# Kernel tuning notes

Hardware: AMD Instinct MI355X
Metric: run time of the kernel (lower is better)

The kernel has to match this reference:

```python
import jax, jax.numpy as jnp
import numpy as np

IN_FEATS = 602
N_HIDDEN = 256
N_CLASSES = 41
N_SRC0 = 292864   # block-1 src nodes (2-hop neighborhood)
N_DST0 = 11264    # block-1 dst == block-0 src (1-hop neighborhood)
N_DST1 = 1024     # seeds
FAN0 = 25         # neighbors per dst in block applied by layer 0
FAN1 = 10         # neighbors per dst in block applied by layer 1


def setup_inputs() -> dict:
    key = jax.random.key(0)
    ks = jax.random.split(key, 9)
    x = jax.random.normal(ks[0], (N_SRC0, IN_FEATS), dtype=jnp.float32)
    src_idx0 = jax.random.randint(ks[1], (N_DST0 * FAN0,), 0, N_SRC0)
    src_idx1 = jax.random.randint(ks[2], (N_DST1 * FAN1,), 0, N_DST0)
    s0 = 1.0 / np.sqrt(IN_FEATS)
    s1 = 1.0 / np.sqrt(N_HIDDEN)
    W_self0 = jax.random.uniform(ks[3], (IN_FEATS, N_HIDDEN), jnp.float32, -s0, s0)
    W_neigh0 = jax.random.uniform(ks[4], (IN_FEATS, N_HIDDEN), jnp.float32, -s0, s0)
    b0 = jnp.zeros((N_HIDDEN,), jnp.float32)
    W_self1 = jax.random.uniform(ks[5], (N_HIDDEN, N_CLASSES), jnp.float32, -s1, s1)
    W_neigh1 = jax.random.uniform(ks[6], (N_HIDDEN, N_CLASSES), jnp.float32, -s1, s1)
    b1 = jnp.zeros((N_CLASSES,), jnp.float32)
    return {"x": x, "W_self0": W_self0, "W_neigh0": W_neigh0, "b0": b0,
            "W_self1": W_self1, "W_neigh1": W_neigh1, "b1": b1,
            "src_idx0": src_idx0, "src_idx1": src_idx1}


def _sage_layer(h_src, h_dst, src_idx, fanout, W_self, W_neigh, b):
    # mean aggregation over exactly `fanout` sampled neighbors per dst node
    n_dst = h_dst.shape[0]
    h_neigh = h_src[src_idx].reshape(n_dst, fanout, -1).mean(axis=1)
    return h_dst @ W_self + h_neigh @ W_neigh + b


def reference(x, W_self0, W_neigh0, b0, W_self1, W_neigh1, b1, src_idx0, src_idx1):
    # layer 0: [N_SRC0, in] -> [N_DST0, hidden], relu; dropout is identity (eval mode)
    h = jax.nn.relu(_sage_layer(x, x[:N_DST0], src_idx0, FAN0, W_self0, W_neigh0, b0))
    # layer 1: [N_DST0, hidden] -> [N_DST1, classes], no activation
    out = _sage_layer(h, h[:N_DST1], src_idx1, FAN1, W_self1, W_neigh1, b1)
    return out
```

## Files before the change

kernel.cpp:

```cpp
#include <hip/hip_runtime.h>
#include <hip/hip_bf16.h>

#define IN_FEATS 602
#define N_HIDDEN 256
#define N_CLASSES 41
#define N_SRC0 292864
#define N_DST0 11264
#define N_DST1 1024
#define FAN0 25
#define FAN1 10
#define KPAD 1216

typedef __attribute__((ext_vector_type(4))) float f32x4;
typedef __attribute__((ext_vector_type(8))) short bf16x8;

static __device__ __forceinline__ unsigned pack_bf16x2(float lo, float hi) {
    unsigned a = __float_as_uint(lo);
    unsigned b = __float_as_uint(hi);
    a = (a + 0x7fffu + ((a >> 16) & 1u)) >> 16;
    b = (b + 0x7fffu + ((b >> 16) & 1u)) >> 16;
    return (a & 0xffffu) | (b << 16);
}

__global__ __launch_bounds__(256) void agg0_kernel(
    const float* __restrict__ x,
    const int* __restrict__ idx,
    __hip_bfloat16* __restrict__ A)
{
    const int wave = threadIdx.x >> 6;
    const int lane = threadIdx.x & 63;
    const int d = blockIdx.x * 4 + wave;

    __shared__ int sidx[4][FAN0];
    if (lane < FAN0) sidx[wave][lane] = idx[d * FAN0 + lane];
    __syncthreads();

    unsigned* Arow = (unsigned*)(A + (size_t)d * KPAD);
    const float* xself = x + (size_t)d * IN_FEATS;

    if (lane < 6) Arow[602 + lane] = 0u;

    float accx[5], accy[5];
    #pragma unroll
    for (int c = 0; c < 5; ++c) { accx[c] = 0.f; accy[c] = 0.f; }

    #pragma unroll 5
    for (int n = 0; n < FAN0; ++n) {
        const float* xr = x + (size_t)sidx[wave][n] * IN_FEATS;
        #pragma unroll
        for (int c = 0; c < 5; ++c) {
            const int f = c * 128 + lane * 2;
            if (f < IN_FEATS) {
                const float2 v = *(const float2*)&xr[f];
                accx[c] += v.x; accy[c] += v.y;
            }
        }
    }

    #pragma unroll
    for (int c = 0; c < 5; ++c) {
        const int f = c * 128 + lane * 2;
        if (f < IN_FEATS) {
            const int f2 = f >> 1;
            const float2 sv = *(const float2*)&xself[f];
            Arow[f2] = pack_bf16x2(sv.x, sv.y);
            *(unsigned*)((char*)Arow + 1204 + f2 * 4) =
                pack_bf16x2(accx[c] * (1.0f / FAN0), accy[c] * (1.0f / FAN0));
        }
    }
}

__global__ __launch_bounds__(256) void wprep_kernel(
    const float* __restrict__ Ws,
    const float* __restrict__ Wn,
    __hip_bfloat16* __restrict__ Wt)
{
    __shared__ float tile[32][33];
    const int k0 = blockIdx.x * 32, n0 = blockIdx.y * 32;
    const int tx = threadIdx.x & 31, ty = threadIdx.x >> 5;

    #pragma unroll
    for (int i = 0; i < 4; ++i) {
        const int k = k0 + ty + i * 8;
        const int n = n0 + tx;
        float v = 0.f;
        if (k < IN_FEATS)            v = Ws[(size_t)k * N_HIDDEN + n];
        else if (k < 2 * IN_FEATS)   v = Wn[(size_t)(k - IN_FEATS) * N_HIDDEN + n];
        tile[ty + i * 8][tx] = v;
    }
    __syncthreads();
    #pragma unroll
    for (int i = 0; i < 4; ++i) {
        const int n = n0 + ty + i * 8;
        const int k = k0 + tx;
        Wt[(size_t)n * KPAD + k] = __float2bfloat16(tile[tx][ty + i * 8]);
    }
}

#define BKK 64
#define LDSW 72

__global__ __launch_bounds__(256) void gemm0_mfma(
    const __hip_bfloat16* __restrict__ A,
    const __hip_bfloat16* __restrict__ Wt,
    const float* __restrict__ bias,
    float* __restrict__ h)
{
    __shared__ __hip_bfloat16 As[64 * LDSW];
    __shared__ __hip_bfloat16 Bs[64 * LDSW];

    const int tid  = threadIdx.x;
    const int lane = tid & 63;
    const int wave = tid >> 6;
    const int wm = wave >> 1, wn = wave & 1;
    const int g = lane >> 4, r = lane & 15;
    const int m0 = blockIdx.y * 64, n0 = blockIdx.x * 64;

    const int srow = tid >> 2;
    const int sc   = (tid & 3) * 16;

    const size_t a_off = (size_t)(m0 + srow) * KPAD + sc;
    const size_t b_off = (size_t)(n0 + srow) * KPAD + sc;

    f32x4 acc[2][2] = {};

    for (int k0 = 0; k0 < KPAD; k0 += BKK) {
        *(float4*)&As[srow * LDSW + sc]     = *(const float4*)&A[a_off + k0];
        *(float4*)&As[srow * LDSW + sc + 8] = *(const float4*)&A[a_off + k0 + 8];
        *(float4*)&Bs[srow * LDSW + sc]     = *(const float4*)&Wt[b_off + k0];
        *(float4*)&Bs[srow * LDSW + sc + 8] = *(const float4*)&Wt[b_off + k0 + 8];
        __syncthreads();

        #pragma unroll
        for (int kh = 0; kh < 2; ++kh) {
            const bf16x8 af0 = *(const bf16x8*)&As[(wm * 32 +      r) * LDSW + kh * 32 + g * 8];
            const bf16x8 af1 = *(const bf16x8*)&As[(wm * 32 + 16 + r) * LDSW + kh * 32 + g * 8];
            const bf16x8 bf0 = *(const bf16x8*)&Bs[(wn * 32 +      r) * LDSW + kh * 32 + g * 8];
            const bf16x8 bf1 = *(const bf16x8*)&Bs[(wn * 32 + 16 + r) * LDSW + kh * 32 + g * 8];

            acc[0][0] = __builtin_amdgcn_mfma_f32_16x16x32_bf16(af0, bf0, acc[0][0], 0, 0, 0);
            acc[0][1] = __builtin_amdgcn_mfma_f32_16x16x32_bf16(af0, bf1, acc[0][1], 0, 0, 0);
            acc[1][0] = __builtin_amdgcn_mfma_f32_16x16x32_bf16(af1, bf0, acc[1][0], 0, 0, 0);
            acc[1][1] = __builtin_amdgcn_mfma_f32_16x16x32_bf16(af1, bf1, acc[1][1], 0, 0, 0);
        }
        __syncthreads();
    }

    #pragma unroll
    for (int mh = 0; mh < 2; ++mh)
        #pragma unroll
        for (int nh = 0; nh < 2; ++nh) {
            const int col = n0 + wn * 32 + nh * 16 + r;
            const float bv = bias[col];
            #pragma unroll
            for (int j = 0; j < 4; ++j) {
                const int row = m0 + wm * 32 + mh * 16 + g * 4 + j;
                const float v = acc[mh][nh][j] + bv;
                h[(size_t)row * N_HIDDEN + col] = fmaxf(v, 0.f);
            }
        }
}

__global__ __launch_bounds__(256) void tail_kernel(
    const float* __restrict__ h,
    const int* __restrict__ idx1,
    const float* __restrict__ Ws,
    const float* __restrict__ Wn,
    const float* __restrict__ b,
    float* __restrict__ out)
{
    const int w = threadIdx.x >> 6;
    const int lane = threadIdx.x & 63;
    const int d = blockIdx.x * 4 + w;

    __shared__ float hd[4][N_HIDDEN];
    __shared__ float hn[4][N_HIDDEN];
    __shared__ int sidx[4][FAN1];
    if (lane < FAN1) sidx[w][lane] = idx1[d * FAN1 + lane];
    __syncthreads();

    {
        const int k0 = lane * 4;
        const float4 self = *(const float4*)&h[(size_t)d * N_HIDDEN + k0];
        float ax = 0.f, ay = 0.f, az = 0.f, aw = 0.f;
        #pragma unroll
        for (int i = 0; i < FAN1; ++i) {
            const float4 v = *(const float4*)&h[(size_t)sidx[w][i] * N_HIDDEN + k0];
            ax += v.x; ay += v.y; az += v.z; aw += v.w;
        }
        *(float4*)&hd[w][k0] = self;
        hn[w][k0 + 0] = ax * (1.0f / FAN1);
        hn[w][k0 + 1] = ay * (1.0f / FAN1);
        hn[w][k0 + 2] = az * (1.0f / FAN1);
        hn[w][k0 + 3] = aw * (1.0f / FAN1);
    }
    __syncthreads();

    if (lane < N_CLASSES) {
        const int n = lane;
        float a0 = b[n], a1 = 0.f, a2 = 0.f, a3 = 0.f;
        #pragma unroll 4
        for (int k = 0; k < N_HIDDEN; k += 4) {
            a0 += hd[w][k + 0] * Ws[(k + 0) * N_CLASSES + n] + hn[w][k + 0] * Wn[(k + 0) * N_CLASSES + n];
            a1 += hd[w][k + 1] * Ws[(k + 1) * N_CLASSES + n] + hn[w][k + 1] * Wn[(k + 1) * N_CLASSES + n];
            a2 += hd[w][k + 2] * Ws[(k + 2) * N_CLASSES + n] + hn[w][k + 2] * Wn[(k + 2) * N_CLASSES + n];
            a3 += hd[w][k + 3] * Ws[(k + 3) * N_CLASSES + n] + hn[w][k + 3] * Wn[(k + 3) * N_CLASSES + n];
        }
        out[(size_t)d * N_CLASSES + n] = a0 + a1 + a2 + a3;
    }
}

extern "C" void kernel_launch(void* const* d_in, const int* in_sizes, int n_in,
                              void* d_out, int out_size, void* d_ws, size_t ws_size,
                              hipStream_t stream) {
    const float* x       = (const float*)d_in[0];
    const float* Wself0  = (const float*)d_in[1];
    const float* Wneigh0 = (const float*)d_in[2];
    const float* b0      = (const float*)d_in[3];
    const float* Wself1  = (const float*)d_in[4];
    const float* Wneigh1 = (const float*)d_in[5];
    const float* b1      = (const float*)d_in[6];
    const int*   idx0    = (const int*)d_in[7];
    const int*   idx1    = (const int*)d_in[8];
    float* out = (float*)d_out;

    __hip_bfloat16* Abf = (__hip_bfloat16*)d_ws;
    __hip_bfloat16* Wt  = Abf + (size_t)N_DST0 * KPAD;
    float*          h   = (float*)(Wt + (size_t)N_HIDDEN * KPAD);

    wprep_kernel<<<dim3(KPAD / 32, N_HIDDEN / 32), 256, 0, stream>>>(Wself0, Wneigh0, Wt);
    agg0_kernel<<<N_DST0 / 4, 256, 0, stream>>>(x, idx0, Abf);
    gemm0_mfma<<<dim3(N_HIDDEN / 64, N_DST0 / 64), 256, 0, stream>>>(Abf, Wt, b0, h);
    tail_kernel<<<N_DST1 / 4, 256, 0, stream>>>(h, idx1, Wself1, Wneigh1, b1, out);
}
```

Before: 232.2 us.

## Merge weight prep into aggregation launch and double-buffer GEMM LDS tiles

Folds the weight transpose/convert kernel into the aggregation kernel as extra blocks, saving one launch and letting both run concurrently. The GEMM switches to double-buffered LDS with register prefetch of the next K tile, which drops one barrier per iteration and overlaps global loads with MFMA work. It also remaps the 1D block index so consecutive blocks share A row tiles across the N columns, aiming for better L2 reuse. The cost is double the LDS footprint and more registers in the GEMM.

```diff
diff --git a/kernel.cpp b/kernel.cpp
--- a/kernel.cpp
+++ b/kernel.cpp
@@ -10,6 +10,8 @@
 #define FAN0 25
 #define FAN1 10
 #define KPAD 1216
+#define NAGG (N_DST0 / 4)
+#define NWP ((KPAD / 32) * (N_HIDDEN / 32))
 
 typedef __attribute__((ext_vector_type(4))) float f32x4;
 typedef __attribute__((ext_vector_type(8))) short bf16x8;
@@ -22,78 +24,81 @@
     return (a & 0xffffu) | (b << 16);
 }
 
-__global__ __launch_bounds__(256) void agg0_kernel(
+__global__ __launch_bounds__(256) void prep_kernel(
     const float* __restrict__ x,
     const int* __restrict__ idx,
-    __hip_bfloat16* __restrict__ A)
+    const float* __restrict__ Ws,
+    const float* __restrict__ Wn,
+    __hip_bfloat16* __restrict__ A,
+    __hip_bfloat16* __restrict__ Wt)
 {
-    const int wave = threadIdx.x >> 6;
-    const int lane = threadIdx.x & 63;
-    const int d = blockIdx.x * 4 + wave;
-
-    __shared__ int sidx[4][FAN0];
-    if (lane < FAN0) sidx[wave][lane] = idx[d * FAN0 + lane];
-    __syncthreads();
-
-    unsigned* Arow = (unsigned*)(A + (size_t)d * KPAD);
-    const float* xself = x + (size_t)d * IN_FEATS;
-
-    if (lane < 6) Arow[602 + lane] = 0u;
-
-    float accx[5], accy[5];
-    #pragma unroll
-    for (int c = 0; c < 5; ++c) { accx[c] = 0.f; accy[c] = 0.f; }
-
-    #pragma unroll 5
-    for (int n = 0; n < FAN0; ++n) {
-        const float* xr = x + (size_t)sidx[wave][n] * IN_FEATS;
+    __shared__ __align__(16) char sm[32 * 33 * 4];
+
+    if (blockIdx.x < NAGG) {
+        int (*sidx)[FAN0] = (int(*)[FAN0])sm;
+        const int wave = threadIdx.x >> 6;
+        const int lane = threadIdx.x & 63;
+        const int d = blockIdx.x * 4 + wave;
+
+        if (lane < FAN0) sidx[wave][lane] = idx[d * FAN0 + lane];
+        __syncthreads();
+
+        unsigned* Arow = (unsigned*)(A + (size_t)d * KPAD);
+        const float* xself = x + (size_t)d * IN_FEATS;
+
+        if (lane < 6) Arow[602 + lane] = 0u;
+
+        float accx[5], accy[5];
+        #pragma unroll
+        for (int c = 0; c < 5; ++c) { accx[c] = 0.f; accy[c] = 0.f; }
+
+        #pragma unroll 5
+        for (int n = 0; n < FAN0; ++n) {
+            const float* xr = x + (size_t)sidx[wave][n] * IN_FEATS;
+            #pragma unroll
+            for (int c = 0; c < 5; ++c) {
+                const int f = c * 128 + lane * 2;
+                if (f < IN_FEATS) {
+                    const float2 v = *(const float2*)&xr[f];
+                    accx[c] += v.x; accy[c] += v.y;
+                }
+            }
+        }
+
         #pragma unroll
         for (int c = 0; c < 5; ++c) {
             const int f = c * 128 + lane * 2;
             if (f < IN_FEATS) {
-                const float2 v = *(const float2*)&xr[f];
-                accx[c] += v.x; accy[c] += v.y;
+                const int f2 = f >> 1;
+                const float2 sv = *(const float2*)&xself[f];
+                Arow[f2] = pack_bf16x2(sv.x, sv.y);
+                *(unsigned*)((char*)Arow + 1204 + f2 * 4) =
+                    pack_bf16x2(accx[c] * (1.0f / FAN0), accy[c] * (1.0f / FAN0));
             }
         }
-    }
-
-    #pragma unroll
-    for (int c = 0; c < 5; ++c) {
-        const int f = c * 128 + lane * 2;
-        if (f < IN_FEATS) {
-            const int f2 = f >> 1;
-            const float2 sv = *(const float2*)&xself[f];
-            Arow[f2] = pack_bf16x2(sv.x, sv.y);
-            *(unsigned*)((char*)Arow + 1204 + f2 * 4) =
-                pack_bf16x2(accx[c] * (1.0f / FAN0), accy[c] * (1.0f / FAN0));
-        }
-    }
-}
-
-__global__ __launch_bounds__(256) void wprep_kernel(
-    const float* __restrict__ Ws,
-    const float* __restrict__ Wn,
-    __hip_bfloat16* __restrict__ Wt)
-{
-    __shared__ float tile[32][33];
-    const int k0 = blockIdx.x * 32, n0 = blockIdx.y * 32;
-    const int tx = threadIdx.x & 31, ty = threadIdx.x >> 5;
-
-    #pragma unroll
-    for (int i = 0; i < 4; ++i) {
-        const int k = k0 + ty + i * 8;
-        const int n = n0 + tx;
-        float v = 0.f;
-        if (k < IN_FEATS)            v = Ws[(size_t)k * N_HIDDEN + n];
-        else if (k < 2 * IN_FEATS)   v = Wn[(size_t)(k - IN_FEATS) * N_HIDDEN + n];
-        tile[ty + i * 8][tx] = v;
-    }
-    __syncthreads();
-    #pragma unroll
-    for (int i = 0; i < 4; ++i) {
-        const int n = n0 + ty + i * 8;
-        const int k = k0 + tx;
-        Wt[(size_t)n * KPAD + k] = __float2bfloat16(tile[tx][ty + i * 8]);
+    } else {
+        float (*tile)[33] = (float(*)[33])sm;
+        const int b = blockIdx.x - NAGG;
+        const int k0 = (b % (KPAD / 32)) * 32;
+        const int n0 = (b / (KPAD / 32)) * 32;
+        const int tx = threadIdx.x & 31, ty = threadIdx.x >> 5;
+
+        #pragma unroll
+        for (int i = 0; i < 4; ++i) {
+            const int k = k0 + ty + i * 8;
+            const int n = n0 + tx;
+            float v = 0.f;
+            if (k < IN_FEATS)            v = Ws[(size_t)k * N_HIDDEN + n];
+            else if (k < 2 * IN_FEATS)   v = Wn[(size_t)(k - IN_FEATS) * N_HIDDEN + n];
+            tile[ty + i * 8][tx] = v;
+        }
+        __syncthreads();
+        #pragma unroll
+        for (int i = 0; i < 4; ++i) {
+            const int n = n0 + ty + i * 8;
+            const int k = k0 + tx;
+            Wt[(size_t)n * KPAD + k] = __float2bfloat16(tile[tx][ty + i * 8]);
+        }
     }
 }
 
@@ -106,44 +111,66 @@
     const float* __restrict__ bias,
     float* __restrict__ h)
 {
-    __shared__ __hip_bfloat16 As[64 * LDSW];
-    __shared__ __hip_bfloat16 Bs[64 * LDSW];
+    __shared__ __hip_bfloat16 As[2][64 * LDSW];
+    __shared__ __hip_bfloat16 Bs[2][64 * LDSW];
+
+    const int D = blockIdx.x;
+    const int s = D & 7;
+    const int e = D >> 3;
+    const int bx = e & 3;
+    const int by = 8 * (e >> 2) + s;
 
     const int tid  = threadIdx.x;
     const int lane = tid & 63;
     const int wave = tid >> 6;
     const int wm = wave >> 1, wn = wave & 1;
     const int g = lane >> 4, r = lane & 15;
-    const int m0 = blockIdx.y * 64, n0 = blockIdx.x * 64;
+    const int m0 = by * 64, n0 = bx * 64;
 
     const int srow = tid >> 2;
     const int sc   = (tid & 3) * 16;
+    const int sbase = srow * LDSW + sc;
 
     const size_t a_off = (size_t)(m0 + srow) * KPAD + sc;
     const size_t b_off = (size_t)(n0 + srow) * KPAD + sc;
 
     f32x4 acc[2][2] = {};
 
-    for (int k0 = 0; k0 < KPAD; k0 += BKK) {
-        *(float4*)&As[srow * LDSW + sc]     = *(const float4*)&A[a_off + k0];
-        *(float4*)&As[srow * LDSW + sc + 8] = *(const float4*)&A[a_off + k0 + 8];
-        *(float4*)&Bs[srow * LDSW + sc]     = *(const float4*)&Wt[b_off + k0];
-        *(float4*)&Bs[srow * LDSW + sc + 8] = *(const float4*)&Wt[b_off + k0 + 8];
+    float4 ra0, ra1, rb0, rb1;
+    ra0 = *(const float4*)&A[a_off];      ra1 = *(const float4*)&A[a_off + 8];
+    rb0 = *(const float4*)&Wt[b_off];     rb1 = *(const float4*)&Wt[b_off + 8];
+    *(float4*)&As[0][sbase] = ra0;  *(float4*)&As[0][sbase + 8] = ra1;
+    *(float4*)&Bs[0][sbase] = rb0;  *(float4*)&Bs[0][sbase + 8] = rb1;
+
+    const int NT = KPAD / BKK;
+    for (int t = 0; t < NT; ++t) {
         __syncthreads();
+        const int cur = t & 1;
+
+        if (t + 1 < NT) {
+            const size_t k1 = (size_t)(t + 1) * BKK;
+            ra0 = *(const float4*)&A[a_off + k1];      ra1 = *(const float4*)&A[a_off + k1 + 8];
+            rb0 = *(const float4*)&Wt[b_off + k1];     rb1 = *(const float4*)&Wt[b_off + k1 + 8];
+        }
 
         #pragma unroll
         for (int kh = 0; kh < 2; ++kh) {
-            const bf16x8 af0 = *(const bf16x8*)&As[(wm * 32 +      r) * LDSW + kh * 32 + g * 8];
-            const bf16x8 af1 = *(const bf16x8*)&As[(wm * 32 + 16 + r) * LDSW + kh * 32 + g * 8];
-            const bf16x8 bf0 = *(const bf16x8*)&Bs[(wn * 32 +      r) * LDSW + kh * 32 + g * 8];
-            const bf16x8 bf1 = *(const bf16x8*)&Bs[(wn * 32 + 16 + r) * LDSW + kh * 32 + g * 8];
+            const bf16x8 af0 = *(const bf16x8*)&As[cur][(wm * 32 +      r) * LDSW + kh * 32 + g * 8];
+            const bf16x8 af1 = *(const bf16x8*)&As[cur][(wm * 32 + 16 + r) * LDSW + kh * 32 + g * 8];
+            const bf16x8 bf0 = *(const bf16x8*)&Bs[cur][(wn * 32 +      r) * LDSW + kh * 32 + g * 8];
+            const bf16x8 bf1 = *(const bf16x8*)&Bs[cur][(wn * 32 + 16 + r) * LDSW + kh * 32 + g * 8];
 
             acc[0][0] = __builtin_amdgcn_mfma_f32_16x16x32_bf16(af0, bf0, acc[0][0], 0, 0, 0);
             acc[0][1] = __builtin_amdgcn_mfma_f32_16x16x32_bf16(af0, bf1, acc[0][1], 0, 0, 0);
             acc[1][0] = __builtin_amdgcn_mfma_f32_16x16x32_bf16(af1, bf0, acc[1][0], 0, 0, 0);
             acc[1][1] = __builtin_amdgcn_mfma_f32_16x16x32_bf16(af1, bf1, acc[1][1], 0, 0, 0);
         }
-        __syncthreads();
+
+        if (t + 1 < NT) {
+            const int nxt = cur ^ 1;
+            *(float4*)&As[nxt][sbase] = ra0;  *(float4*)&As[nxt][sbase + 8] = ra1;
+            *(float4*)&Bs[nxt][sbase] = rb0;  *(float4*)&Bs[nxt][sbase + 8] = rb1;
+        }
     }
 
     #pragma unroll
@@ -228,8 +255,7 @@
     __hip_bfloat16* Wt  = Abf + (size_t)N_DST0 * KPAD;
     float*          h   = (float*)(Wt + (size_t)N_HIDDEN * KPAD);
 
-    wprep_kernel<<<dim3(KPAD / 32, N_HIDDEN / 32), 256, 0, stream>>>(Wself0, Wneigh0, Wt);
-    agg0_kernel<<<N_DST0 / 4, 256, 0, stream>>>(x, idx0, Abf);
-    gemm0_mfma<<<dim3(N_HIDDEN / 64, N_DST0 / 64), 256, 0, stream>>>(Abf, Wt, b0, h);
+    prep_kernel<<<NAGG + NWP, 256, 0, stream>>>(x, idx0, Wself0, Wneigh0, Abf, Wt);
+    gemm0_mfma<<<(N_HIDDEN / 64) * (N_DST0 / 64), 256, 0, stream>>>(Abf, Wt, b0, h);
     tail_kernel<<<N_DST1 / 4, 256, 0, stream>>>(h, idx1, Wself1, Wneigh1, b1, out);
 }
```

Result: faster. 214.8 us (-7.5%).
